# Optimization experiments

Measured on AMD Instinct MI355X. Metric: run time of the kernel, lower is better.

## Reference

```python
import jax, jax.numpy as jnp
import numpy as np

R_CUT = 10.0
ROUNDS = 1  # num_message_passing_rounds


def setup_inputs() -> dict:
    key = jax.random.key(0)
    N, DEG, S, NRBF, G = 10000, 16, 128, 20, 64
    E = N * DEG
    ks = jax.random.split(key, 16)
    w = lambda k, shp, fan: (jax.random.normal(k, shp, dtype=jnp.float32) / np.float32(np.sqrt(fan)))
    return {
        "edge_vector_diffs": jax.random.normal(ks[0], (E, 3), dtype=jnp.float32) * 3.0,
        "edge_lengths": jax.random.uniform(ks[1], (E,), dtype=jnp.float32) * 15.0,
        "node_from": jnp.repeat(jnp.arange(N), DEG),            # every node has DEG outgoing edges
        "node_graph_index": jax.random.randint(ks[2], (N,), 0, G),
        "num_graphs": G,
        "emb0": jax.random.normal(ks[3], (S,), dtype=jnp.float32) * 0.01,  # embedding.weight[0]
        "phi_w1": w(ks[4], (S, S), S), "phi_b1": jnp.zeros((S,), jnp.float32),
        "phi_w2": w(ks[5], (S, 3 * S), S), "phi_b2": jnp.zeros((3 * S,), jnp.float32),
        "filt_w": w(ks[6], (NRBF, 3 * S), NRBF), "filt_b": jnp.zeros((3 * S,), jnp.float32),
        "u_w": w(ks[7], (S, S), S), "v_w": w(ks[8], (S, S), S),
        "upd_w1": w(ks[9], (2 * S, S), 2 * S), "upd_b1": jnp.zeros((S,), jnp.float32),
        "upd_w2": w(ks[10], (S, 3 * S), S), "upd_b2": jnp.zeros((3 * S,), jnp.float32),
        "out_w1": w(ks[11], (S, S), S), "out_b1": jnp.zeros((S,), jnp.float32),
        "out_w2": w(ks[12], (S, 1), S), "out_b2": jnp.zeros((1,), jnp.float32),
    }


def reference(edge_vector_diffs, edge_lengths, node_from, node_graph_index, num_graphs,
              emb0, phi_w1, phi_b1, phi_w2, phi_b2, filt_w, filt_b, u_w, v_w,
              upd_w1, upd_b1, upd_w2, upd_b2, out_w1, out_b1, out_w2, out_b2):
    S = phi_w1.shape[0]
    N = node_graph_index.shape[0]
    NRBF = filt_w.shape[0]
    silu = jax.nn.silu
    seg = lambda v, n: jax.ops.segment_sum(v, node_from, num_segments=n)

    mask = (jnp.abs(edge_lengths) <= R_CUT).astype(jnp.float32)          # [E] nbr_mask
    r = jnp.linalg.norm(edge_vector_diffs, axis=1)                        # [E]
    r_safe = jnp.maximum(r, 1e-12)
    k = jnp.arange(1, NRBF + 1, dtype=jnp.float32)
    # PAINN sinc radial basis sin(k*pi*r/r_cut)/r, then linear -> [E, 3S]
    rbf = jnp.sin(k[None, :] * jnp.pi * r_safe[:, None] / R_CUT) / r_safe[:, None]
    cutoff = 0.5 * (jnp.cos(jnp.pi * r / R_CUT) + 1.0) * (r < R_CUT)      # cosine cutoff
    W = (rbf @ filt_w + filt_b) * cutoff[:, None]                          # [E, 3S]

    tile3 = jnp.arange(S) % 3  # xyzxyz... truncation pattern from .repeat(...)[: S]
    # scalar Frobenius norm of each node's masked neighbor-diff block
    frob = jnp.sqrt(seg(mask * r * r, N))                                  # [N]
    denom_e = frob[node_from]
    denom_e = jnp.where(denom_e > 0, denom_e, 1.0)
    normalized = edge_vector_diffs / denom_e[:, None]                      # [E, 3]
    norm_exp = normalized[:, tile3]                                        # [E, S]

    # state init: sum over dim 1 of embedding(zeros) == S * embedding.weight[0]
    state = jnp.broadcast_to(jnp.float32(S) * emb0, (N, S))
    state_vec = jnp.zeros((N, 3, S), jnp.float32)

    for _ in range(ROUNDS):
        # message block (nbrs_node_from == destination node, so sync update == original sequential loop)
        phi = silu(state[node_from] @ phi_w1 + phi_b1) @ phi_w2 + phi_b2   # [E, 3S]
        prod = phi * W
        m1, m2, m3 = prod[:, :S], prod[:, S:2 * S], prod[:, 2 * S:]
        vec_msg = state_vec[node_from] * m1[:, None, :] + (norm_exp * m3)[:, None, :]  # [E,3,S]
        state = seg(m2 * mask[:, None], N)                                 # [N, S]
        state_vec = seg(vec_msg * mask[:, None, None], N)                  # [N, 3, S]
        # update block
        U = jnp.einsum('nps,st->npt', state_vec, u_w)                      # [N,3,S]
        V = jnp.einsum('nps,st->npt', state_vec, v_w)
        UV = jnp.einsum('nps,nqs->npq', U, V)                              # [N,3,3]
        Vnorm = jnp.sqrt(jnp.sum(V * V, axis=1))                           # [N,S]
        a = silu(jnp.concatenate([Vnorm, state], axis=-1) @ upd_w1 + upd_b1) @ upd_w2 + upd_b2
        a_vv, a_sv, a_ss = a[:, :S], a[:, S:2 * S], a[:, 2 * S:]
        uv_tiled = jnp.sum(UV, axis=1)[:, tile3]                           # [N,S]
        state = a_ss + uv_tiled * a_sv
        state_vec = U * a_vv[:, None, :]

    graph_state = jax.ops.segment_sum(state, node_graph_index, num_segments=num_graphs)
    out = (silu(graph_state @ out_w1 + out_b1) @ out_w2 + out_b2).ravel()  # [num_graphs]
    return out
```

## Files before the change

### kernel.cpp

```cpp
#include <hip/hip_runtime.h>
#include <math.h>

#define NN   10000
#define DEG  16
#define SS   128
#define NRBF 20
#define GG   64
#define RC   10.0f
#define PI_F 3.14159265358979323846f
#define NB   8

__device__ __forceinline__ float silu_f(float x){
    return x / (1.0f + __expf(-x));
}

__global__ __launch_bounds__(256) void k_phi1(
    const float* __restrict__ emb0,
    const float* __restrict__ w1, const float* __restrict__ b1,
    float* __restrict__ phiH, float* __restrict__ gs){
    __shared__ float s0[SS];
    __shared__ float part[2][SS];
    int t = threadIdx.x;
    for (int i = t; i < GG*SS; i += 256) gs[i] = 0.0f;
    if (t < SS) s0[t] = 128.0f * emb0[t];
    __syncthreads();
    int c = t & 127, half = t >> 7;
    float acc = 0.0f;
    int s0i = half * 64;
    #pragma unroll 8
    for (int s = 0; s < 64; s++)
        acc = fmaf(s0[s0i + s], w1[(s0i + s)*SS + c], acc);
    part[half][c] = acc;
    __syncthreads();
    if (t < SS) phiH[t] = silu_f(b1[t] + part[0][t] + part[1][t]);
}

__global__ __launch_bounds__(128) void k_phi2(
    const float* __restrict__ phiH,
    const float* __restrict__ w2, const float* __restrict__ b2,
    float* __restrict__ phiW){
    __shared__ float hL[SS];
    __shared__ float part[4][32];
    int t = threadIdx.x;
    hL[t] = phiH[t];
    __syncthreads();
    int c  = blockIdx.x*32 + (t & 31);
    int kk = t >> 5;
    float acc = 0.0f;
    int sbase = kk * 32;
    #pragma unroll 8
    for (int s = 0; s < 32; s++)
        acc = fmaf(hL[sbase + s], w2[(sbase + s)*3*SS + c], acc);
    part[kk][t & 31] = acc;
    __syncthreads();
    if (t < 32){
        int cc = blockIdx.x*32 + t;
        phiW[cc] = b2[cc] + part[0][t] + part[1][t] + part[2][t] + part[3][t];
    }
}

__global__ __launch_bounds__(128) void k_edge(
    const float* __restrict__ evd, const float* __restrict__ elen,
    const int* __restrict__ node_from,
    const float* __restrict__ filt_w, const float* __restrict__ filt_b,
    const float* __restrict__ phiW,
    float* __restrict__ state, float* __restrict__ sv){
    __shared__ float rS[DEG];
    __shared__ float mcL[DEG];
    __shared__ float frL[DEG];
    __shared__ float eV[DEG][3];
    __shared__ float rbfL[DEG][NRBF];
    __shared__ float invD;
    int n = blockIdx.x;
    int t = threadIdx.x;

    if (t < DEG){
        int e = n*DEG + t;
        float x = evd[3*e+0], y = evd[3*e+1], z = evd[3*e+2];
        float r = sqrtf(x*x + y*y + z*z);
        float len  = elen[e];
        float mask = (fabsf(len) <= RC) ? 1.0f : 0.0f;
        float cut  = (r < RC) ? 0.5f*(cosf(PI_F*r*(1.0f/RC)) + 1.0f) : 0.0f;
        rS[t]  = fmaxf(r, 1e-12f);
        mcL[t] = mask * cut;
        frL[t] = mask * r * r;
        eV[t][0] = x; eV[t][1] = y; eV[t][2] = z;
    }
    __syncthreads();
    for (int idx = t; idx < DEG*NRBF; idx += 128){
        int e = idx / NRBF, k = idx % NRBF;
        float rs = rS[e];
        rbfL[e][k] = sinf((float)(k+1) * (PI_F/RC) * rs) / rs;
    }
    if (t == 0){
        float s = 0.0f;
        for (int e = 0; e < DEG; e++) s += frL[e];
        float fbn = sqrtf(s);
        invD = (fbn > 0.0f) ? 1.0f/fbn : 1.0f;
    }
    __syncthreads();

    int gc1 = SS + t;
    int gc2 = 2*SS + t;
    float fw1[NRBF], fw2[NRBF];
    #pragma unroll
    for (int k = 0; k < NRBF; k++){
        fw1[k] = filt_w[k*(3*SS) + gc1];
        fw2[k] = filt_w[k*(3*SS) + gc2];
    }
    float fb1 = filt_b[gc1], fb2 = filt_b[gc2];
    float ph1 = phiW[gc1],   ph2 = phiW[gc2];
    float iD  = invD;
    int   s3  = t % 3;

    float acc1 = 0.0f, acc2 = 0.0f;
    for (int e = 0; e < DEG; e++){
        float mc = mcL[e];
        if (mc == 0.0f) continue;
        const float4* rv = (const float4*)(&rbfL[e][0]);
        float4 r0 = rv[0], r1 = rv[1], r2 = rv[2], r3 = rv[3], r4 = rv[4];
        float rr[20] = {r0.x,r0.y,r0.z,r0.w, r1.x,r1.y,r1.z,r1.w,
                        r2.x,r2.y,r2.z,r2.w, r3.x,r3.y,r3.z,r3.w,
                        r4.x,r4.y,r4.z,r4.w};
        float w1 = fb1, w2 = fb2;
        #pragma unroll
        for (int k = 0; k < NRBF; k++){
            w1 = fmaf(rr[k], fw1[k], w1);
            w2 = fmaf(rr[k], fw2[k], w2);
        }
        acc1 = fmaf(ph1*mc, w1, acc1);
        acc2 = fmaf(ph2*mc*eV[e][s3]*iD, w2, acc2);
    }
    int nf = node_from[n*DEG];
    state[nf*SS + t] = acc1;
    sv[nf*SS + t]    = acc2;
}

__global__ __launch_bounds__(128) void k_update(
    const float* __restrict__ state, const float* __restrict__ sv,
    const float* __restrict__ u_w, const float* __restrict__ v_w,
    const float* __restrict__ upd_w1, const float* __restrict__ upd_b1,
    const float* __restrict__ upd_w2, const float* __restrict__ upd_b2,
    const int* __restrict__ ngi, float* __restrict__ gs){
    __shared__ float svT[SS][NB];
    __shared__ float xT[2*SS][NB];
    __shared__ float h2T[SS][NB];
    __shared__ float red[2][NB];
    __shared__ float dL[NB];
    int t  = threadIdx.x;
    int n0 = blockIdx.x * NB;

    for (int idx = t; idx < NB*SS; idx += 128){
        int b = idx >> 7, s = idx & (SS-1);
        svT[s][b]     = sv[(n0+b)*SS + s];
        xT[SS+s][b]   = state[(n0+b)*SS + s];
    }
    __syncthreads();

    float accU[NB], accV[NB];
    #pragma unroll
    for (int b = 0; b < NB; b++){ accU[b]=0.f; accV[b]=0.f; }
    for (int s = 0; s < SS; s++){
        float wu = u_w[s*SS + t];
        float wv = v_w[s*SS + t];
        const float4* sp = (const float4*)(&svT[s][0]);
        float4 s03 = sp[0], s47 = sp[1];
        float svv[NB] = {s03.x,s03.y,s03.z,s03.w,s47.x,s47.y,s47.z,s47.w};
        #pragma unroll
        for (int b = 0; b < NB; b++){
            accU[b] = fmaf(svv[b], wu, accU[b]);
            accV[b] = fmaf(svv[b], wv, accV[b]);
        }
    }

    int lane = t & 63, wid = t >> 6;
    #pragma unroll
    for (int b = 0; b < NB; b++){
        float p = accU[b]*accV[b];
        for (int off = 32; off; off >>= 1) p += __shfl_down(p, off);
        if (lane == 0) red[wid][b] = p;
    }
    {
        float4 q0, q1;
        q0.x = sqrtf(3.f*accV[0]*accV[0]); q0.y = sqrtf(3.f*accV[1]*accV[1]);
        q0.z = sqrtf(3.f*accV[2]*accV[2]); q0.w = sqrtf(3.f*accV[3]*accV[3]);
        q1.x = sqrtf(3.f*accV[4]*accV[4]); q1.y = sqrtf(3.f*accV[5]*accV[5]);
        q1.z = sqrtf(3.f*accV[6]*accV[6]); q1.w = sqrtf(3.f*accV[7]*accV[7]);
        ((float4*)(&xT[t][0]))[0] = q0;
        ((float4*)(&xT[t][0]))[1] = q1;
    }
    __syncthreads();
    if (t < NB) dL[t] = red[0][t] + red[1][t];

    float accH[NB];
    #pragma unroll
    for (int b = 0; b < NB; b++) accH[b] = 0.f;
    for (int i = 0; i < 2*SS; i++){
        float w = upd_w1[i*SS + t];
        const float4* xp = (const float4*)(&xT[i][0]);
        float4 x03 = xp[0], x47 = xp[1];
        float xv[NB] = {x03.x,x03.y,x03.z,x03.w,x47.x,x47.y,x47.z,x47.w};
        #pragma unroll
        for (int b = 0; b < NB; b++) accH[b] = fmaf(xv[b], w, accH[b]);
    }
    float b1v = upd_b1[t];
    {
        float4 q0, q1;
        q0.x = silu_f(accH[0]+b1v); q0.y = silu_f(accH[1]+b1v);
        q0.z = silu_f(accH[2]+b1v); q0.w = silu_f(accH[3]+b1v);
        q1.x = silu_f(accH[4]+b1v); q1.y = silu_f(accH[5]+b1v);
        q1.z = silu_f(accH[6]+b1v); q1.w = silu_f(accH[7]+b1v);
        ((float4*)(&h2T[t][0]))[0] = q0;
        ((float4*)(&h2T[t][0]))[1] = q1;
    }
    __syncthreads();

    float a1[NB], a2[NB];
    #pragma unroll
    for (int b = 0; b < NB; b++){ a1[b]=0.f; a2[b]=0.f; }
    for (int j = 0; j < SS; j++){
        float w1 = upd_w2[j*3*SS + SS   + t];
        float w2 = upd_w2[j*3*SS + 2*SS + t];
        const float4* hp = (const float4*)(&h2T[j][0]);
        float4 h03 = hp[0], h47 = hp[1];
        float hv[NB] = {h03.x,h03.y,h03.z,h03.w,h47.x,h47.y,h47.z,h47.w};
        #pragma unroll
        for (int b = 0; b < NB; b++){
            a1[b] = fmaf(hv[b], w1, a1[b]);
            a2[b] = fmaf(hv[b], w2, a2[b]);
        }
    }
    float bsv = upd_b2[SS+t], bss = upd_b2[2*SS+t];
    #pragma unroll
    for (int b = 0; b < NB; b++){
        float ns = (a2[b] + bss) + 3.0f*dL[b]*(a1[b] + bsv);
        int g = ngi[n0+b];
        atomicAdd(&gs[g*SS + t], ns);
    }
}

__global__ __launch_bounds__(128) void k_out(
    const float* __restrict__ gs,
    const float* __restrict__ w1, const float* __restrict__ b1,
    const float* __restrict__ w2, const float* __restrict__ b2,
    float* __restrict__ out){
    __shared__ float gsL[SS];
    __shared__ float red[2];
    int g = blockIdx.x, t = threadIdx.x;
    gsL[t] = gs[g*SS + t];
    __syncthreads();
    float acc = b1[t];
    #pragma unroll 4
    for (int s = 0; s < SS; s++) acc = fmaf(gsL[s], w1[s*SS + t], acc);
    float p = silu_f(acc) * w2[t];
    for (int off = 32; off; off >>= 1) p += __shfl_down(p, off);
    if ((t & 63) == 0) red[t >> 6] = p;
    __syncthreads();
    if (t == 0) out[g] = red[0] + red[1] + b2[0];
}

extern "C" void kernel_launch(void* const* d_in, const int* in_sizes, int n_in,
                              void* d_out, int out_size, void* d_ws, size_t ws_size,
                              hipStream_t stream) {
    const float* evd     = (const float*)d_in[0];
    const float* elen    = (const float*)d_in[1];
    const int*   nfrom   = (const int*)  d_in[2];
    const int*   ngi     = (const int*)  d_in[3];
    const float* emb0    = (const float*)d_in[5];
    const float* phi_w1  = (const float*)d_in[6];
    const float* phi_b1  = (const float*)d_in[7];
    const float* phi_w2  = (const float*)d_in[8];
    const float* phi_b2  = (const float*)d_in[9];
    const float* filt_w  = (const float*)d_in[10];
    const float* filt_b  = (const float*)d_in[11];
    const float* u_w     = (const float*)d_in[12];
    const float* v_w     = (const float*)d_in[13];
    const float* upd_w1  = (const float*)d_in[14];
    const float* upd_b1  = (const float*)d_in[15];
    const float* upd_w2  = (const float*)d_in[16];
    const float* upd_b2  = (const float*)d_in[17];
    const float* out_w1  = (const float*)d_in[18];
    const float* out_b1  = (const float*)d_in[19];
    const float* out_w2  = (const float*)d_in[20];
    const float* out_b2  = (const float*)d_in[21];

    float* ws    = (float*)d_ws;
    float* phiW  = ws;
    float* state = ws + 512;
    float* sv    = state + NN*SS;
    float* gs    = sv + NN*SS;
    float* phiH  = gs + GG*SS;

    k_phi1<<<1, 256, 0, stream>>>(emb0, phi_w1, phi_b1, phiH, gs);
    k_phi2<<<12, 128, 0, stream>>>(phiH, phi_w2, phi_b2, phiW);
    k_edge<<<NN, 128, 0, stream>>>(evd, elen, nfrom, filt_w, filt_b, phiW, state, sv);
    k_update<<<NN/NB, 128, 0, stream>>>(state, sv, u_w, v_w,
                                        upd_w1, upd_b1, upd_w2, upd_b2, ngi, gs);
    k_out<<<GG, 128, 0, stream>>>(gs, out_w1, out_b1, out_w2, out_b2, (float*)d_out);
}
```

Measured before the change: 184.2 us.

## Stage update-kernel weights through LDS with register-prefetched double buffering

In k_update, the three matrix-multiply phases no longer read per-row weights directly from global memory inside the inner loop. Weight tiles of 16 rows are now loaded into shared memory with float4 loads, and the next tile is prefetched into registers while the current one is being consumed. The goal is to hide global load latency and vectorize the weight fetches. The cost is extra LDS usage, two barriers per tile, and more registers, which may lower occupancy.

```diff
diff --git a/kernel.cpp b/kernel.cpp
--- a/kernel.cpp
+++ b/kernel.cpp
@@ -9,6 +9,7 @@
 #define RC   10.0f
 #define PI_F 3.14159265358979323846f
 #define NB   8
+#define TS   16
 
 __device__ __forceinline__ float silu_f(float x){
     return x / (1.0f + __expf(-x));
@@ -142,6 +143,8 @@
     const float* __restrict__ upd_w1, const float* __restrict__ upd_b1,
     const float* __restrict__ upd_w2, const float* __restrict__ upd_b2,
     const int* __restrict__ ngi, float* __restrict__ gs){
+    __shared__ float wA[TS*SS];
+    __shared__ float wB[TS*SS];
     __shared__ float svT[SS][NB];
     __shared__ float xT[2*SS][NB];
     __shared__ float h2T[SS][NB];
@@ -152,25 +155,47 @@
 
     for (int idx = t; idx < NB*SS; idx += 128){
         int b = idx >> 7, s = idx & (SS-1);
-        svT[s][b]     = sv[(n0+b)*SS + s];
-        xT[SS+s][b]   = state[(n0+b)*SS + s];
-    }
-    __syncthreads();
+        svT[s][b]   = sv[(n0+b)*SS + s];
+        xT[SS+s][b] = state[(n0+b)*SS + s];
+    }
+
+    float4* wA4 = (float4*)wA;
+    float4* wB4 = (float4*)wB;
+
+    const float4* ug = (const float4*)u_w;
+    const float4* vg = (const float4*)v_w;
+    float4 pa0 = ug[t], pa1 = ug[t+128], pa2 = ug[t+256], pa3 = ug[t+384];
+    float4 pb0 = vg[t], pb1 = vg[t+128], pb2 = vg[t+256], pb3 = vg[t+384];
 
     float accU[NB], accV[NB];
     #pragma unroll
     for (int b = 0; b < NB; b++){ accU[b]=0.f; accV[b]=0.f; }
-    for (int s = 0; s < SS; s++){
-        float wu = u_w[s*SS + t];
-        float wv = v_w[s*SS + t];
-        const float4* sp = (const float4*)(&svT[s][0]);
-        float4 s03 = sp[0], s47 = sp[1];
-        float svv[NB] = {s03.x,s03.y,s03.z,s03.w,s47.x,s47.y,s47.z,s47.w};
-        #pragma unroll
-        for (int b = 0; b < NB; b++){
-            accU[b] = fmaf(svv[b], wu, accU[b]);
-            accV[b] = fmaf(svv[b], wv, accV[b]);
-        }
+
+    for (int s0 = 0; s0 < SS; s0 += TS){
+        wA4[t] = pa0; wA4[t+128] = pa1; wA4[t+256] = pa2; wA4[t+384] = pa3;
+        wB4[t] = pb0; wB4[t+128] = pb1; wB4[t+256] = pb2; wB4[t+384] = pb3;
+        if (s0 + TS < SS){
+            int base = (s0 + TS)*(SS/4);
+            pa0 = ug[base+t]; pa1 = ug[base+t+128];
+            pa2 = ug[base+t+256]; pa3 = ug[base+t+384];
+            pb0 = vg[base+t]; pb1 = vg[base+t+128];
+            pb2 = vg[base+t+256]; pb3 = vg[base+t+384];
+        }
+        __syncthreads();
+        #pragma unroll
+        for (int s = 0; s < TS; s++){
+            float wu = wA[s*SS + t];
+            float wv = wB[s*SS + t];
+            const float4* sp = (const float4*)(&svT[s0+s][0]);
+            float4 s03 = sp[0], s47 = sp[1];
+            float svv[NB] = {s03.x,s03.y,s03.z,s03.w,s47.x,s47.y,s47.z,s47.w};
+            #pragma unroll
+            for (int b = 0; b < NB; b++){
+                accU[b] = fmaf(svv[b], wu, accU[b]);
+                accV[b] = fmaf(svv[b], wv, accV[b]);
+            }
+        }
+        __syncthreads();
     }
 
     int lane = t & 63, wid = t >> 6;
@@ -192,16 +217,45 @@
     __syncthreads();
     if (t < NB) dL[t] = red[0][t] + red[1][t];
 
+    const float4* w1g = (const float4*)upd_w1;
+    {
+        pa0 = w1g[t];     pa1 = w1g[t+128]; pa2 = w1g[t+256]; pa3 = w1g[t+384];
+        pb0 = w1g[t+512]; pb1 = w1g[t+640]; pb2 = w1g[t+768]; pb3 = w1g[t+896];
+    }
     float accH[NB];
     #pragma unroll
     for (int b = 0; b < NB; b++) accH[b] = 0.f;
-    for (int i = 0; i < 2*SS; i++){
-        float w = upd_w1[i*SS + t];
-        const float4* xp = (const float4*)(&xT[i][0]);
-        float4 x03 = xp[0], x47 = xp[1];
-        float xv[NB] = {x03.x,x03.y,x03.z,x03.w,x47.x,x47.y,x47.z,x47.w};
-        #pragma unroll
-        for (int b = 0; b < NB; b++) accH[b] = fmaf(xv[b], w, accH[b]);
+
+    for (int i0 = 0; i0 < 2*SS; i0 += 2*TS){
+        wA4[t] = pa0; wA4[t+128] = pa1; wA4[t+256] = pa2; wA4[t+384] = pa3;
+        wB4[t] = pb0; wB4[t+128] = pb1; wB4[t+256] = pb2; wB4[t+384] = pb3;
+        if (i0 + 2*TS < 2*SS){
+            int base = (i0 + 2*TS)*(SS/4);
+            pa0 = w1g[base+t];     pa1 = w1g[base+t+128];
+            pa2 = w1g[base+t+256]; pa3 = w1g[base+t+384];
+            pb0 = w1g[base+t+512]; pb1 = w1g[base+t+640];
+            pb2 = w1g[base+t+768]; pb3 = w1g[base+t+896];
+        }
+        __syncthreads();
+        #pragma unroll
+        for (int s = 0; s < TS; s++){
+            float w = wA[s*SS + t];
+            const float4* xp = (const float4*)(&xT[i0+s][0]);
+            float4 x03 = xp[0], x47 = xp[1];
+            float xv[NB] = {x03.x,x03.y,x03.z,x03.w,x47.x,x47.y,x47.z,x47.w};
+            #pragma unroll
+            for (int b = 0; b < NB; b++) accH[b] = fmaf(xv[b], w, accH[b]);
+        }
+        #pragma unroll
+        for (int s = 0; s < TS; s++){
+            float w = wB[s*SS + t];
+            const float4* xp = (const float4*)(&xT[i0+TS+s][0]);
+            float4 x03 = xp[0], x47 = xp[1];
+            float xv[NB] = {x03.x,x03.y,x03.z,x03.w,x47.x,x47.y,x47.z,x47.w};
+            #pragma unroll
+            for (int b = 0; b < NB; b++) accH[b] = fmaf(xv[b], w, accH[b]);
+        }
+        __syncthreads();
     }
     float b1v = upd_b1[t];
     {
@@ -213,23 +267,49 @@
         ((float4*)(&h2T[t][0]))[0] = q0;
         ((float4*)(&h2T[t][0]))[1] = q1;
     }
-    __syncthreads();
-
+
+    const float4* w2g = (const float4*)upd_w2;
+    int r0q = t >> 5,          c4 = t & 31;
+    int r1q = (t+128) >> 5;
+    int r2q = (t+256) >> 5;
+    int r3q = (t+384) >> 5;
+    {
+        pa0 = w2g[r0q*96 + 32 + c4]; pa1 = w2g[r1q*96 + 32 + c4];
+        pa2 = w2g[r2q*96 + 32 + c4]; pa3 = w2g[r3q*96 + 32 + c4];
+        pb0 = w2g[r0q*96 + 64 + c4]; pb1 = w2g[r1q*96 + 64 + c4];
+        pb2 = w2g[r2q*96 + 64 + c4]; pb3 = w2g[r3q*96 + 64 + c4];
+    }
     float a1[NB], a2[NB];
     #pragma unroll
     for (int b = 0; b < NB; b++){ a1[b]=0.f; a2[b]=0.f; }
-    for (int j = 0; j < SS; j++){
-        float w1 = upd_w2[j*3*SS + SS   + t];
-        float w2 = upd_w2[j*3*SS + 2*SS + t];
-        const float4* hp = (const float4*)(&h2T[j][0]);
-        float4 h03 = hp[0], h47 = hp[1];
-        float hv[NB] = {h03.x,h03.y,h03.z,h03.w,h47.x,h47.y,h47.z,h47.w};
-        #pragma unroll
-        for (int b = 0; b < NB; b++){
-            a1[b] = fmaf(hv[b], w1, a1[b]);
-            a2[b] = fmaf(hv[b], w2, a2[b]);
-        }
-    }
+
+    for (int j0 = 0; j0 < SS; j0 += TS){
+        wA4[t] = pa0; wA4[t+128] = pa1; wA4[t+256] = pa2; wA4[t+384] = pa3;
+        wB4[t] = pb0; wB4[t+128] = pb1; wB4[t+256] = pb2; wB4[t+384] = pb3;
+        if (j0 + TS < SS){
+            int jb = j0 + TS;
+            pa0 = w2g[(jb+r0q)*96 + 32 + c4]; pa1 = w2g[(jb+r1q)*96 + 32 + c4];
+            pa2 = w2g[(jb+r2q)*96 + 32 + c4]; pa3 = w2g[(jb+r3q)*96 + 32 + c4];
+            pb0 = w2g[(jb+r0q)*96 + 64 + c4]; pb1 = w2g[(jb+r1q)*96 + 64 + c4];
+            pb2 = w2g[(jb+r2q)*96 + 64 + c4]; pb3 = w2g[(jb+r3q)*96 + 64 + c4];
+        }
+        __syncthreads();
+        #pragma unroll
+        for (int s = 0; s < TS; s++){
+            float wa = wA[s*SS + t];
+            float wb = wB[s*SS + t];
+            const float4* hp = (const float4*)(&h2T[j0+s][0]);
+            float4 h03 = hp[0], h47 = hp[1];
+            float hv[NB] = {h03.x,h03.y,h03.z,h03.w,h47.x,h47.y,h47.z,h47.w};
+            #pragma unroll
+            for (int b = 0; b < NB; b++){
+                a1[b] = fmaf(hv[b], wa, a1[b]);
+                a2[b] = fmaf(hv[b], wb, a2[b]);
+            }
+        }
+        __syncthreads();
+    }
+
     float bsv = upd_b2[SS+t], bss = upd_b2[2*SS+t];
     #pragma unroll
     for (int b = 0; b < NB; b++){
```

Result: slower. 199.8 us (+8.4%).
